# Optimization experiments

Hardware: AMD Instinct MI355X
Metric: run time of the kernel (lower is better)

Reference implementation:

```python
import jax, jax.numpy as jnp
import numpy as np

AREA = 4
HEADS = 8

def conv1x1(x, W, b):
    # x: [B,C,H,W], W: [O,C], b: [O]
    return jnp.einsum('bchw,oc->bohw', x, W) + b[None, :, None, None]

def dwconv5(x, W, b):
    # depthwise 5x5, pad 2, groups = C; W: [C,1,5,5]
    C = x.shape[1]
    y = jax.lax.conv_general_dilated(
        x, W, window_strides=(1, 1), padding=[(2, 2), (2, 2)],
        dimension_numbers=('NCHW', 'OIHW', 'NCHW'), feature_group_count=C)
    return y + b[None, :, None, None]

def setup_inputs() -> dict:
    key = jax.random.key(0)
    ks = jax.random.split(key, 9)
    B, C, H, W = 4, 256, 64, 64
    s = 0.05
    return {
        'x': jax.random.normal(ks[0], (B, C, H, W), jnp.float32),
        'Wqk': jax.random.normal(ks[1], (2 * C, C), jnp.float32) * s,
        'bqk': jax.random.normal(ks[2], (2 * C,), jnp.float32) * s,
        'Wv': jax.random.normal(ks[3], (C, C), jnp.float32) * s,
        'bv': jax.random.normal(ks[4], (C,), jnp.float32) * s,
        'Wpe': jax.random.normal(ks[5], (C, 1, 5, 5), jnp.float32) * s,
        'bpe': jax.random.normal(ks[6], (C,), jnp.float32) * s,
        'Wproj': jax.random.normal(ks[7], (C, C), jnp.float32) * s,
        'bproj': jax.random.normal(ks[8], (C,), jnp.float32) * s,
    }

def reference(x, Wqk, bqk, Wv, bv, Wpe, bpe, Wproj, bproj):
    B, C, H, W = x.shape
    N = H * W
    hd = C // HEADS
    # qk / v projections (1x1 conv + folded BN bias, no activation)
    qk = conv1x1(x, Wqk, bqk).reshape(B, 2 * C, N).transpose(0, 2, 1)  # [B,N,2C]
    v4 = conv1x1(x, Wv, bv)                                            # [B,C,H,W]
    pp = dwconv5(v4, Wpe, bpe)                                         # positional enc
    v = v4.reshape(B, C, N).transpose(0, 2, 1)                         # [B,N,C]
    # area split: [B*area, N/area, .]
    Ba, Na = B * AREA, N // AREA
    qk = qk.reshape(Ba, Na, 2 * C)
    v = v.reshape(Ba, Na, C)
    q, k = qk[..., :C], qk[..., C:]
    q = q.reshape(Ba, Na, HEADS, hd)
    k = k.reshape(Ba, Na, HEADS, hd)
    v = v.reshape(Ba, Na, HEADS, hd)
    # manual softmax attention: (q^T k) * d^-0.5 -> softmax -> weight v
    attn = jnp.einsum('bqhd,bkhd->bhqk', q, k) * (hd ** -0.5)
    attn = jax.nn.softmax(attn, axis=-1)
    out = jnp.einsum('bhqk,bkhd->bqhd', attn, v)                       # [Ba,Na,H,hd]
    # merge areas back and go to NCHW
    out = out.reshape(B, N, C).reshape(B, H, W, C).transpose(0, 3, 1, 2)
    return conv1x1(out + pp, Wproj, bproj)
```

## Files before the change

### kernel.cpp

```cpp
#include <hip/hip_runtime.h>

typedef unsigned short u16;
typedef unsigned int u32;
using f32x4  = __attribute__((ext_vector_type(4))) float;
using u32x2  = __attribute__((ext_vector_type(2))) u32;
using u32x4  = __attribute__((ext_vector_type(4))) u32;
using bf16x8 = __attribute__((ext_vector_type(8))) short;

__device__ __forceinline__ u16 f2b(float f) {
  union { float f; u32 u; } v; v.f = f;
  return (u16)((v.u + 0x7FFFu + ((v.u >> 16) & 1u)) >> 16);
}
__device__ __forceinline__ float b2f(u16 u) {
  union { u32 u; float f; } v; v.u = ((u32)u) << 16;
  return v.f;
}
__device__ __forceinline__ u32 pk2(float a, float b) {
  u32 r;
  asm("v_cvt_pk_bf16_f32 %0, %1, %2" : "=v"(r) : "v"(a), "v"(b));
  return r;
}

__global__ __launch_bounds__(256) void kconvert(
    const float* __restrict__ Wqk, const float* __restrict__ Wv,
    const float* __restrict__ Wproj, u16* __restrict__ dst) {
  int e = (blockIdx.x * 256 + threadIdx.x) * 4;
  f32x4 v;
  if (e < 131072)      v = *(const f32x4*)(Wqk + e);
  else if (e < 196608) v = *(const f32x4*)(Wv + (e - 131072));
  else                 v = *(const f32x4*)(Wproj + (e - 196608));
  u32* d = (u32*)(dst + e);
  d[0] = (u32)f2b(v[0]) | ((u32)f2b(v[1]) << 16);
  d[1] = (u32)f2b(v[2]) | ((u32)f2b(v[3]) << 16);
}

__global__ __launch_bounds__(256) void kqkv(
    const float* __restrict__ x,
    const u16* __restrict__ Wqk_bf, const float* __restrict__ bqk,
    const u16* __restrict__ Wv_bf,  const float* __restrict__ bv,
    u16* __restrict__ qk_tm, u16* __restrict__ v_cm) {
  __shared__ __align__(16) u16 xs[64 * 264];
  const int bid = blockIdx.x;
  const int b   = bid >> 6;
  const int n0  = (bid & 63) * 64;
  const int tid = threadIdx.x;

  {
    const int part = tid & 15, cr = tid >> 4;
    #pragma unroll
    for (int p = 0; p < 16; ++p) {
      const int c = p * 16 + cr;
      f32x4 v = *(const f32x4*)(x + (size_t)(b * 256 + c) * 4096 + n0 + part * 4);
      const int t0 = part * 4;
      xs[(t0 + 0) * 264 + c] = f2b(v[0]);
      xs[(t0 + 1) * 264 + c] = f2b(v[1]);
      xs[(t0 + 2) * 264 + c] = f2b(v[2]);
      xs[(t0 + 3) * 264 + c] = f2b(v[3]);
    }
  }
  __syncthreads();

  const int wave = tid >> 6, l = tid & 63, lg = l & 15, lq = l >> 4;

  for (int ot = wave; ot < 48; ot += 4) {
    if (ot < 32) {
      bf16x8 bfr[8];
      const u16* wrow = Wqk_bf + (ot * 16 + lg) * 256 + lq * 8;
      #pragma unroll
      for (int kk = 0; kk < 8; ++kk) bfr[kk] = *(const bf16x8*)(wrow + kk * 32);
      const float bias = bqk[ot * 16 + lg];
      #pragma unroll
      for (int ts = 0; ts < 4; ++ts) {
        f32x4 acc = {0.f, 0.f, 0.f, 0.f};
        #pragma unroll
        for (int kk = 0; kk < 8; ++kk) {
          bf16x8 af = *(const bf16x8*)(&xs[(ts * 16 + lg) * 264 + kk * 32 + lq * 8]);
          acc = __builtin_amdgcn_mfma_f32_16x16x32_bf16(af, bfr[kk], acc, 0, 0, 0);
        }
        u16* dst = qk_tm + (size_t)(b * 4096 + n0 + ts * 16 + lq * 4) * 512 + ot * 16 + lg;
        #pragma unroll
        for (int r = 0; r < 4; ++r) dst[(size_t)r * 512] = f2b(acc[r] + bias);
      }
    } else {
      const int o2 = ot - 32;
      bf16x8 afw[8];
      const u16* wrow = Wv_bf + (o2 * 16 + lg) * 256 + lq * 8;
      #pragma unroll
      for (int kk = 0; kk < 8; ++kk) afw[kk] = *(const bf16x8*)(wrow + kk * 32);
      float bvr[4];
      #pragma unroll
      for (int r = 0; r < 4; ++r) bvr[r] = bv[o2 * 16 + lq * 4 + r];
      #pragma unroll
      for (int ts = 0; ts < 4; ++ts) {
        f32x4 acc = {0.f, 0.f, 0.f, 0.f};
        #pragma unroll
        for (int kk = 0; kk < 8; ++kk) {
          bf16x8 bfx = *(const bf16x8*)(&xs[(ts * 16 + lg) * 264 + kk * 32 + lq * 8]);
          acc = __builtin_amdgcn_mfma_f32_16x16x32_bf16(afw[kk], bfx, acc, 0, 0, 0);
        }
        #pragma unroll
        for (int r = 0; r < 4; ++r) {
          const int o = o2 * 16 + lq * 4 + r;
          v_cm[(size_t)(b * 256 + o) * 4096 + n0 + ts * 16 + lg] = f2b(acc[r] + bvr[r]);
        }
      }
    }
  }
}

__global__ __launch_bounds__(256) void kdw(
    const u16* __restrict__ v_cm, const float* __restrict__ Wpe,
    const float* __restrict__ bpe, u16* __restrict__ pp) {
  __shared__ __align__(16) u16 vsh[5 * 64 * 64];
  __shared__ float wsh[64 * 25];
  const int bid = blockIdx.x;
  const int ct = bid & 3, h = (bid >> 2) & 63, b = bid >> 8;
  const int c0 = ct * 64;
  const int tid = threadIdx.x;

  for (int i = tid; i < 64 * 25; i += 256) wsh[i] = Wpe[(c0 + i / 25) * 25 + i % 25];
  #pragma unroll
  for (int uu = 0; uu < 10; ++uu) {
    const int u = uu * 256 + tid;
    const int dy = u >> 9, rem = u & 511, c = rem >> 3, part = rem & 7;
    const int hy = h + dy - 2;
    u32x4 val = {0, 0, 0, 0};
    if (hy >= 0 && hy < 64)
      val = *(const u32x4*)(v_cm + (size_t)(b * 256 + c0 + c) * 4096 + hy * 64 + part * 8);
    *(u32x4*)(&vsh[(dy * 64 + c) * 64 + part * 8]) = val;
  }
  __syncthreads();

  const int c = tid >> 2, w0 = (tid & 3) * 16;
  float acc16[16];
  const float bias = bpe[c0 + c];
  #pragma unroll
  for (int i = 0; i < 16; ++i) acc16[i] = bias;
  const float* wc = &wsh[c * 25];
  #pragma unroll
  for (int dy = 0; dy < 5; ++dy) {
    const u16* row = &vsh[(dy * 64 + c) * 64];
    float rowv[20];
    #pragma unroll
    for (int j = 0; j < 20; ++j) {
      const int ww = w0 + j - 2;
      rowv[j] = (ww >= 0 && ww < 64) ? b2f(row[ww]) : 0.f;
    }
    #pragma unroll
    for (int dx = 0; dx < 5; ++dx) {
      const float wv = wc[dy * 5 + dx];
      #pragma unroll
      for (int wi = 0; wi < 16; ++wi) acc16[wi] += rowv[wi + dx] * wv;
    }
  }
  u32x4 o0, o1;
  #pragma unroll
  for (int i = 0; i < 4; ++i)
    o0[i] = (u32)f2b(acc16[2 * i]) | ((u32)f2b(acc16[2 * i + 1]) << 16);
  #pragma unroll
  for (int i = 0; i < 4; ++i)
    o1[i] = (u32)f2b(acc16[8 + 2 * i]) | ((u32)f2b(acc16[9 + 2 * i]) << 16);
  u16* dst = pp + (size_t)(b * 256 + c0 + c) * 4096 + h * 64 + w0;
  *(u32x4*)(dst) = o0;
  *(u32x4*)(dst + 8) = o1;
}

__global__ __launch_bounds__(256) void kattn(
    const u16* __restrict__ qk_tm, const u16* __restrict__ v_cm,
    u16* __restrict__ out_tm) {
  __shared__ __align__(16) char pbuf[4][32 * 128];

  const int bid = blockIdx.x;
  const int xcd = bid & 7, idx = bid >> 3;
  const int pair = xcd * 16 + (idx >> 3);
  const int qb = idx & 7;
  const int h = pair & 7, ba = pair >> 3;
  const int b = ba >> 2, area = ba & 3;
  const size_t row_base = (size_t)b * 4096 + area * 1024;

  const int tid = threadIdx.x;
  const int wave = tid >> 6, l = tid & 63, lg = l & 15, lq = l >> 4;
  char* pbc = pbuf[wave];
  const int swz = (lg & 7) << 4;
  const float kscale = 0.25503484f;

  bf16x8 bQ[2];
  #pragma unroll
  for (int s = 0; s < 2; ++s) {
    const size_t qrow = row_base + qb * 128 + wave * 32 + s * 16 + lg;
    bQ[s] = *(const bf16x8*)(qk_tm + qrow * 512 + h * 32 + lq * 8);
  }

  const u16* Kbase = qk_tm + row_base * 512 + 256 + h * 32 + lq * 8;
  const u16* Vbase = v_cm + (size_t)(b * 256 + h * 32) * 4096 + area * 1024 + lq * 8;

  f32x4 accO[2][2];
  float dAcc[2] = {0.f, 0.f};
  #pragma unroll
  for (int s = 0; s < 2; ++s)
    #pragma unroll
    for (int d = 0; d < 2; ++d) accO[s][d] = (f32x4){0.f, 0.f, 0.f, 0.f};

  bf16x8 fK0[4], fV0[4], fK1[4], fV1[4];

  auto LOAD = [&](bf16x8* fK, bf16x8* fV, int kb) {
    #pragma unroll
    for (int t = 0; t < 4; ++t)
      fK[t] = *(const bf16x8*)(Kbase + (size_t)(kb * 64 + t * 16 + lg) * 512);
    #pragma unroll
    for (int kk = 0; kk < 2; ++kk)
      #pragma unroll
      for (int dt = 0; dt < 2; ++dt)
        fV[kk * 2 + dt] = *(const bf16x8*)(Vbase + (size_t)(dt * 16 + lg) * 4096 + kb * 64 + kk * 32);
  };

  auto COMP = [&](bf16x8* fK, bf16x8* fV) {
    f32x4 sc[2][4];
    #pragma unroll
    for (int s = 0; s < 2; ++s)
      #pragma unroll
      for (int t = 0; t < 4; ++t) {
        f32x4 z = {0.f, 0.f, 0.f, 0.f};
        sc[s][t] = __builtin_amdgcn_mfma_f32_16x16x32_bf16(fK[t], bQ[s], z, 0, 0, 0);
      }
    #pragma unroll
    for (int s = 0; s < 2; ++s)
      #pragma unroll
      for (int t = 0; t < 4; ++t) {
        const float e0 = __builtin_amdgcn_exp2f(sc[s][t][0] * kscale);
        const float e1 = __builtin_amdgcn_exp2f(sc[s][t][1] * kscale);
        const float e2 = __builtin_amdgcn_exp2f(sc[s][t][2] * kscale);
        const float e3 = __builtin_amdgcn_exp2f(sc[s][t][3] * kscale);
        dAcc[s] += (e0 + e1) + (e2 + e3);
        u32x2 w = {pk2(e0, e1), pk2(e2, e3)};
        *(u32x2*)(pbc + (s * 16 + lg) * 128 + ((t * 32 + lq * 8) ^ swz)) = w;
      }
    asm volatile("s_waitcnt lgkmcnt(0)" ::: "memory");
    __builtin_amdgcn_sched_barrier(0);
    #pragma unroll
    for (int s = 0; s < 2; ++s)
      #pragma unroll
      for (int kk = 0; kk < 2; ++kk) {
        bf16x8 aP = *(const bf16x8*)(pbc + (s * 16 + lg) * 128 + ((kk * 64 + lq * 16) ^ swz));
        #pragma unroll
        for (int dt = 0; dt < 2; ++dt)
          accO[s][dt] = __builtin_amdgcn_mfma_f32_16x16x32_bf16(aP, fV[kk * 2 + dt], accO[s][dt], 0, 0, 0);
      }
  };

  LOAD(fK0, fV0, 0);
  for (int kb = 0; kb < 16; kb += 2) {
    LOAD(fK1, fV1, kb + 1);
    COMP(fK0, fV0);
    if (kb + 2 < 16) LOAD(fK0, fV0, kb + 2);
    COMP(fK1, fV1);
  }

  #pragma unroll
  for (int s = 0; s < 2; ++s) {
    float d = dAcc[s];
    d += __shfl_xor(d, 16);
    d += __shfl_xor(d, 32);
    #pragma unroll
    for (int r = 0; r < 4; ++r) {
      const float den = __shfl(d, lq * 4 + r);
      const float inv = __builtin_amdgcn_rcpf(den);
      const size_t row = row_base + qb * 128 + wave * 32 + s * 16 + lq * 4 + r;
      u16* dst = out_tm + row * 256 + h * 32 + lg;
      dst[0]  = f2b(accO[s][0][r] * inv);
      dst[16] = f2b(accO[s][1][r] * inv);
    }
  }
}

__global__ __launch_bounds__(256) void kproj(
    const u16* __restrict__ out_tm, const u16* __restrict__ pp,
    const u16* __restrict__ Wproj_bf, const float* __restrict__ bproj,
    float* __restrict__ out) {
  __shared__ __align__(16) u16 as_[64 * 264];
  const int bid = blockIdx.x;
  const int b = bid >> 6;
  const int n0 = (bid & 63) * 64;
  const int tid = threadIdx.x;
  {
    const int r = tid >> 2, qp = tid & 3;
    const u32x4* src = (const u32x4*)(out_tm + (size_t)(b * 4096 + n0 + r) * 256 + qp * 64);
    #pragma unroll
    for (int j = 0; j < 8; ++j)
      *(u32x4*)(&as_[r * 264 + qp * 64 + j * 8]) = src[j];
  }
  __syncthreads();
  {
    const int part = tid & 7;
    #pragma unroll
    for (int pass = 0; pass < 8; ++pass) {
      const int c = pass * 32 + (tid >> 3);
      u32x4 v = *(const u32x4*)(pp + (size_t)(b * 256 + c) * 4096 + n0 + part * 8);
      #pragma unroll
      for (int jj = 0; jj < 4; ++jj) {
        u32 w = v[jj];
        u16* q0 = &as_[(part * 8 + jj * 2) * 264 + c];
        *q0 = f2b(b2f(*q0) + b2f((u16)(w & 0xffffu)));
        u16* q1 = &as_[(part * 8 + jj * 2 + 1) * 264 + c];
        *q1 = f2b(b2f(*q1) + b2f((u16)(w >> 16)));
      }
    }
  }
  __syncthreads();
  const int wave = tid >> 6, l = tid & 63, lg = l & 15, lq = l >> 4;
  #pragma unroll
  for (int oi = 0; oi < 4; ++oi) {
    const int ot = oi * 4 + wave;
    bf16x8 afw[8];
    const u16* wrow = Wproj_bf + (ot * 16 + lg) * 256 + lq * 8;
    #pragma unroll
    for (int kk = 0; kk < 8; ++kk) afw[kk] = *(const bf16x8*)(wrow + kk * 32);
    float bpr[4];
    #pragma unroll
    for (int r = 0; r < 4; ++r) bpr[r] = bproj[ot * 16 + lq * 4 + r];
    #pragma unroll
    for (int ts = 0; ts < 4; ++ts) {
      f32x4 acc = {0.f, 0.f, 0.f, 0.f};
      #pragma unroll
      for (int kk = 0; kk < 8; ++kk) {
        bf16x8 bfx = *(const bf16x8*)(&as_[(ts * 16 + lg) * 264 + kk * 32 + lq * 8]);
        acc = __builtin_amdgcn_mfma_f32_16x16x32_bf16(afw[kk], bfx, acc, 0, 0, 0);
      }
      #pragma unroll
      for (int r = 0; r < 4; ++r) {
        const int o = ot * 16 + lq * 4 + r;
        out[(size_t)(b * 256 + o) * 4096 + n0 + ts * 16 + lg] = acc[r] + bpr[r];
      }
    }
  }
}

extern "C" void kernel_launch(void* const* d_in, const int* in_sizes, int n_in,
                              void* d_out, int out_size, void* d_ws, size_t ws_size,
                              hipStream_t stream) {
  const float* x     = (const float*)d_in[0];
  const float* Wqk   = (const float*)d_in[1];
  const float* bqk   = (const float*)d_in[2];
  const float* Wv    = (const float*)d_in[3];
  const float* bv    = (const float*)d_in[4];
  const float* Wpe   = (const float*)d_in[5];
  const float* bpe   = (const float*)d_in[6];
  const float* Wproj = (const float*)d_in[7];
  const float* bproj = (const float*)d_in[8];
  float* out = (float*)d_out;

  char* ws = (char*)d_ws;
  u16* qk_tm  = (u16*)(ws);
  u16* v_cm   = (u16*)(ws + 16777216);
  u16* pp     = (u16*)(ws + 25165824);
  u16* out_tm = (u16*)(ws + 33554432);
  u16* wbf    = (u16*)(ws + 41943040);
  u16* Wqk_bf = wbf;
  u16* Wv_bf = wbf + 131072;
  u16* Wproj_bf = wbf + 196608;

  kconvert<<<256, 256, 0, stream>>>(Wqk, Wv, Wproj, wbf);
  kqkv<<<256, 256, 0, stream>>>(x, Wqk_bf, bqk, Wv_bf, bv, qk_tm, v_cm);
  kdw<<<1024, 256, 0, stream>>>(v_cm, Wpe, bpe, pp);
  kattn<<<1024, 256, 0, stream>>>(qk_tm, v_cm, out_tm);
  kproj<<<256, 256, 0, stream>>>(out_tm, pp, Wproj_bf, bproj, out);
}
```

Before: 132.4 us.

## Keep softmax probabilities in registers and permute V loads to match

Removes the LDS round-trip for the exponentiated attention scores. The P fragment for the PV MFMA is now packed directly from the score MFMA output registers, and the V loads are permuted (two 8-byte loads at offsets lq*4 and +16) so the k-index ordering matches. This eliminates the LDS writes and reads and the lgkmcnt wait per block. In exchange, V is fetched with narrower 8-byte global loads instead of 16-byte loads.

```diff
diff --git a/kernel.cpp b/kernel.cpp
--- a/kernel.cpp
+++ b/kernel.cpp
@@ -19,6 +19,9 @@
   u32 r;
   asm("v_cvt_pk_bf16_f32 %0, %1, %2" : "=v"(r) : "v"(a), "v"(b));
   return r;
+}
+__device__ __forceinline__ bf16x8 asbf(u32x4 v) {
+  union { u32x4 u; bf16x8 b; } c; c.u = v; return c.b;
 }
 
 __global__ __launch_bounds__(256) void kconvert(
@@ -168,8 +171,6 @@
 __global__ __launch_bounds__(256) void kattn(
     const u16* __restrict__ qk_tm, const u16* __restrict__ v_cm,
     u16* __restrict__ out_tm) {
-  __shared__ __align__(16) char pbuf[4][32 * 128];
-
   const int bid = blockIdx.x;
   const int xcd = bid & 7, idx = bid >> 3;
   const int pair = xcd * 16 + (idx >> 3);
@@ -180,8 +181,6 @@
 
   const int tid = threadIdx.x;
   const int wave = tid >> 6, l = tid & 63, lg = l & 15, lq = l >> 4;
-  char* pbc = pbuf[wave];
-  const int swz = (lg & 7) << 4;
   const float kscale = 0.25503484f;
 
   bf16x8 bQ[2];
@@ -192,7 +191,7 @@
   }
 
   const u16* Kbase = qk_tm + row_base * 512 + 256 + h * 32 + lq * 8;
-  const u16* Vbase = v_cm + (size_t)(b * 256 + h * 32) * 4096 + area * 1024 + lq * 8;
+  const u16* Vbase = v_cm + (size_t)(b * 256 + h * 32) * 4096 + area * 1024 + lq * 4;
 
   f32x4 accO[2][2];
   float dAcc[2] = {0.f, 0.f};
@@ -201,51 +200,55 @@
     #pragma unroll
     for (int d = 0; d < 2; ++d) accO[s][d] = (f32x4){0.f, 0.f, 0.f, 0.f};
 
-  bf16x8 fK0[4], fV0[4], fK1[4], fV1[4];
-
-  auto LOAD = [&](bf16x8* fK, bf16x8* fV, int kb) {
+  bf16x8 fK0[4], fK1[4];
+  u32x4 fV0[4], fV1[4];
+
+  auto LOAD = [&](bf16x8* fK, u32x4* fV, int kb) {
     #pragma unroll
     for (int t = 0; t < 4; ++t)
       fK[t] = *(const bf16x8*)(Kbase + (size_t)(kb * 64 + t * 16 + lg) * 512);
     #pragma unroll
     for (int kk = 0; kk < 2; ++kk)
       #pragma unroll
-      for (int dt = 0; dt < 2; ++dt)
-        fV[kk * 2 + dt] = *(const bf16x8*)(Vbase + (size_t)(dt * 16 + lg) * 4096 + kb * 64 + kk * 32);
+      for (int dt = 0; dt < 2; ++dt) {
+        const u16* p = Vbase + (size_t)(dt * 16 + lg) * 4096 + kb * 64 + kk * 32;
+        u32x2 a = *(const u32x2*)(p);
+        u32x2 c = *(const u32x2*)(p + 16);
+        fV[kk * 2 + dt] = (u32x4){a[0], a[1], c[0], c[1]};
+      }
   };
 
-  auto COMP = [&](bf16x8* fK, bf16x8* fV) {
-    f32x4 sc[2][4];
-    #pragma unroll
-    for (int s = 0; s < 2; ++s)
+  auto COMP = [&](bf16x8* fK, u32x4* fV) {
+    #pragma unroll
+    for (int s = 0; s < 2; ++s) {
+      f32x4 sc[4];
       #pragma unroll
       for (int t = 0; t < 4; ++t) {
         f32x4 z = {0.f, 0.f, 0.f, 0.f};
-        sc[s][t] = __builtin_amdgcn_mfma_f32_16x16x32_bf16(fK[t], bQ[s], z, 0, 0, 0);
-      }
-    #pragma unroll
-    for (int s = 0; s < 2; ++s)
-      #pragma unroll
-      for (int t = 0; t < 4; ++t) {
-        const float e0 = __builtin_amdgcn_exp2f(sc[s][t][0] * kscale);
-        const float e1 = __builtin_amdgcn_exp2f(sc[s][t][1] * kscale);
-        const float e2 = __builtin_amdgcn_exp2f(sc[s][t][2] * kscale);
-        const float e3 = __builtin_amdgcn_exp2f(sc[s][t][3] * kscale);
-        dAcc[s] += (e0 + e1) + (e2 + e3);
-        u32x2 w = {pk2(e0, e1), pk2(e2, e3)};
-        *(u32x2*)(pbc + (s * 16 + lg) * 128 + ((t * 32 + lq * 8) ^ swz)) = w;
-      }
-    asm volatile("s_waitcnt lgkmcnt(0)" ::: "memory");
-    __builtin_amdgcn_sched_barrier(0);
-    #pragma unroll
-    for (int s = 0; s < 2; ++s)
+        sc[t] = __builtin_amdgcn_mfma_f32_16x16x32_bf16(fK[t], bQ[s], z, 0, 0, 0);
+      }
+      float e[4][4];
+      #pragma unroll
+      for (int t = 0; t < 4; ++t)
+        #pragma unroll
+        for (int r = 0; r < 4; ++r)
+          e[t][r] = __builtin_amdgcn_exp2f(sc[t][r] * kscale);
+      #pragma unroll
+      for (int t = 0; t < 4; ++t)
+        dAcc[s] += (e[t][0] + e[t][1]) + (e[t][2] + e[t][3]);
       #pragma unroll
       for (int kk = 0; kk < 2; ++kk) {
-        bf16x8 aP = *(const bf16x8*)(pbc + (s * 16 + lg) * 128 + ((kk * 64 + lq * 16) ^ swz));
+        u32x4 ap = {pk2(e[2 * kk][0],     e[2 * kk][1]),
+                    pk2(e[2 * kk][2],     e[2 * kk][3]),
+                    pk2(e[2 * kk + 1][0], e[2 * kk + 1][1]),
+                    pk2(e[2 * kk + 1][2], e[2 * kk + 1][3])};
+        bf16x8 aP = asbf(ap);
         #pragma unroll
         for (int dt = 0; dt < 2; ++dt)
-          accO[s][dt] = __builtin_amdgcn_mfma_f32_16x16x32_bf16(aP, fV[kk * 2 + dt], accO[s][dt], 0, 0, 0);
-      }
+          accO[s][dt] = __builtin_amdgcn_mfma_f32_16x16x32_bf16(
+              aP, asbf(fV[kk * 2 + dt]), accO[s][dt], 0, 0, 0);
+      }
+    }
   };
 
   LOAD(fK0, fV0, 0);
```

New measurement: 159.6 us. 20.6% more time.
